# Performance work log

Hardware: AMD Instinct MI355X
Metric: run time of the kernel (lower is better)

Reference implementation:

```python
import math
import jax, jax.numpy as jnp
import numpy as np

SCALING = 16.0 / 32.0  # alpha / rank


def real_fourier_orthogonal_multiply(c):
    """Vectorized equivalent of the per-frequency Python loop: build a complex
    spectrum from real Fourier coefficients and inverse-rfft along last dim."""
    n = c.shape[-1]
    sqrt_n = math.sqrt(n)
    pair_scale = math.sqrt(n / 2.0)
    max_f = (n - 1) // 2
    work = c.astype(jnp.float32)
    dc = (work[..., 0] * sqrt_n)[..., None].astype(jnp.complex64)
    cos = work[..., 1:1 + 2 * max_f:2] * pair_scale
    sin = work[..., 2:2 + 2 * max_f:2] * pair_scale
    mid = (cos - 1j * sin).astype(jnp.complex64)  # freqs 1..max_f
    parts = [dc, mid]
    if n % 2 == 0:
        parts.append((work[..., -1] * sqrt_n)[..., None].astype(jnp.complex64))
    spectrum = jnp.concatenate(parts, axis=-1)  # [..., n//2+1]
    return jnp.fft.irfft(spectrum, n=n, axis=-1).astype(c.dtype)


def setup_inputs() -> dict:
    key = jax.random.key(0)
    ks = jax.random.split(key, 9)
    B, S, D_in, D_out, R0, R1, E = 4, 2048, 4096, 4096, 32, 8, 3
    x = jax.random.normal(ks[0], (B, S, D_in), dtype=jnp.float32)
    W_base = jax.random.normal(ks[1], (D_out, D_in), dtype=jnp.float32) * 0.02
    b_base = jax.random.normal(ks[2], (D_out,), dtype=jnp.float32) * 0.02
    enc0 = jax.random.normal(ks[3], (R0, D_in), dtype=jnp.float32) * 0.02
    enc1 = jax.random.normal(ks[4], (R1, D_in), dtype=jnp.float32) * 0.02
    coefs0 = jax.random.normal(ks[5], (E, D_out, R0), dtype=jnp.float32) * 0.02
    coefs1 = jax.random.normal(ks[6], (E, D_out, R1), dtype=jnp.float32) * 0.02
    # sparse decoder masks (buffers in the torch module)
    mask0 = jax.random.randint(ks[7], (E, D_out, R0), 0, 2).astype(bool)
    mask1 = jax.random.randint(ks[8], (E, D_out, R1), 0, 2).astype(bool)
    return dict(x=x, W_base=W_base, b_base=b_base, enc0=enc0, enc1=enc1,
                coefs0=coefs0, coefs1=coefs1, mask0=mask0, mask1=mask1)


def reference(x, W_base, b_base, enc0, enc1, coefs0, coefs1, mask0, mask1):
    # base linear
    base = jnp.einsum('bsd,od->bso', x, W_base) + b_base
    # encoder blocks (shared across experts)
    e0 = jnp.einsum('bsd,rd->bsr', x, enc0)  # [B,S,R0]
    e1 = jnp.einsum('bsd,rd->bsr', x, enc1)  # [B,S,R1]
    # masked decoder blocks per expert, summed over blocks
    w0 = coefs0 * mask0.astype(coefs0.dtype)  # [E,O,R0]
    w1 = coefs1 * mask1.astype(coefs1.dtype)  # [E,O,R1]
    decoded = (jnp.einsum('bsr,eor->ebso', e0, w0)
               + jnp.einsum('bsr,eor->ebso', e1, w1))  # [E,B,S,O]
    transformed = real_fourier_orthogonal_multiply(decoded)
    update = transformed.sum(axis=0)  # sum over active experts
    return base + update * SCALING
```

## Files before the change

kernel.cpp:

```cpp
#include <hip/hip_runtime.h>

typedef __attribute__((ext_vector_type(2))) float f32x2;
typedef __attribute__((ext_vector_type(4))) float f32x4;
typedef __attribute__((ext_vector_type(16))) float f32x16;
typedef __attribute__((ext_vector_type(8))) short bf16x8;
typedef __attribute__((ext_vector_type(8))) unsigned short u16x8;

#define GL2LDS(g, l) __builtin_amdgcn_global_load_lds( \
    (const __attribute__((address_space(1))) void*)(g), \
    (__attribute__((address_space(3))) void*)(l), 16, 0, 0)

__device__ __forceinline__ unsigned short f2bf(float x) {
    union { float f; unsigned u; } v; v.f = x;
    unsigned r = (v.u + 0x7FFF + ((v.u >> 16) & 1)) >> 16;
    return (unsigned short)r;
}

__global__ __launch_bounds__(256) void k_prep(const float* __restrict__ c0,
                                              const float* __restrict__ c1,
                                              const int* __restrict__ m0,
                                              const int* __restrict__ m1,
                                              float* __restrict__ Wc,
                                              const float* __restrict__ x,
                                              unsigned short* __restrict__ xb) {
    int b = blockIdx.x;
    if (b < 640) {
        int idx = b * 256 + threadIdx.x;
        if (idx >= 4096 * 40) return;
        int o = idx / 40, c = idx % 40;
        float s = 0.f;
        if (c < 32) {
            #pragma unroll
            for (int e = 0; e < 3; ++e) {
                int i = (e * 4096 + o) * 32 + c;
                s += c0[i] * (m0[i] != 0 ? 1.f : 0.f);
            }
        } else {
            int r = c - 32;
            #pragma unroll
            for (int e = 0; e < 3; ++e) {
                int i = (e * 4096 + o) * 8 + r;
                s += c1[i] * (m1[i] != 0 ? 1.f : 0.f);
            }
        }
        Wc[idx] = s;
    } else {
        int idx = (b - 640) * 256 + threadIdx.x;
        f32x4 f0 = ((const f32x4*)x)[(size_t)idx * 2];
        f32x4 f1 = ((const f32x4*)x)[(size_t)idx * 2 + 1];
        u16x8 o;
        o[0] = f2bf(f0[0]); o[1] = f2bf(f0[1]); o[2] = f2bf(f0[2]); o[3] = f2bf(f0[3]);
        o[4] = f2bf(f1[0]); o[5] = f2bf(f1[1]); o[6] = f2bf(f1[2]); o[7] = f2bf(f1[3]);
        *(u16x8*)(xb + (size_t)idx * 8) = o;
    }
}

__global__ __launch_bounds__(256) void k_gmat(const float* __restrict__ Wc,
                                              float* __restrict__ G) {
    __shared__ float lds[10752];
    int tid = threadIdx.x;
    int t_base = blockIdx.x * 8;
    int f_slot = tid & 31;
    int tg = (tid >> 5) & 1;
    int rg = tid >> 6;
    float acc[4][10];
    #pragma unroll
    for (int a = 0; a < 4; ++a)
        #pragma unroll
        for (int b = 0; b < 10; ++b) acc[a][b] = 0.f;

    for (int ch = 0; ch < 16; ++ch) {
        __syncthreads();
        #pragma unroll
        for (int j = 0; j < 10; ++j) {
            int idx = tid + j * 256;
            int row = idx / 20;
            int v = idx % 20;
            int f = ch * 128 + row;
            f32x4 val = {0.f, 0.f, 0.f, 0.f};
            if (f >= 1) val = *(const f32x4*)(Wc + (2 * f - 1) * 40 + v * 4);
            *(f32x4*)(lds + row * 84 + v * 4) = val;
        }
        __syncthreads();
        #pragma unroll
        for (int j2 = 0; j2 < 4; ++j2) {
            int f_local = f_slot + 32 * j2;
            int f = ch * 128 + f_local;
            float cs[4], sn[4];
            #pragma unroll
            for (int tt = 0; tt < 4; ++tt) {
                int t = t_base + tg * 4 + tt;
                int ph = (f * t) & 4095;
                float rev = (float)ph * (1.0f / 4096.0f);
                cs[tt] = __builtin_amdgcn_cosf(rev);
                sn[tt] = __builtin_amdgcn_sinf(rev);
            }
            const float* Lc = lds + f_local * 84 + rg * 10;
            const float* Ls = Lc + 40;
            #pragma unroll
            for (int rr = 0; rr < 10; ++rr) {
                float wc = Lc[rr], ws = Ls[rr];
                #pragma unroll
                for (int tt = 0; tt < 4; ++tt)
                    acc[tt][rr] += cs[tt] * wc + sn[tt] * ws;
            }
        }
    }
    __syncthreads();
    #pragma unroll
    for (int tt = 0; tt < 4; ++tt)
        #pragma unroll
        for (int rr = 0; rr < 10; ++rr)
            lds[tid * 40 + tt * 10 + rr] = acc[tt][rr];
    __syncthreads();
    for (int oi = tid; oi < 320; oi += 256) {
        int t_local = oi / 40, rc = oi % 40;
        int tg2 = t_local >> 2, tsub = t_local & 3;
        int rg2 = rc / 10, rsub = rc % 10;
        float s = 0.f;
        #pragma unroll
        for (int fs = 0; fs < 32; ++fs)
            s += lds[(fs + tg2 * 32 + rg2 * 64) * 40 + tsub * 10 + rsub];
        int t = t_base + t_local;
        float dc = Wc[rc];
        float ny = Wc[4095 * 40 + rc];
        float sign = (t & 1) ? -1.f : 1.f;
        float g = 0.5f * (0.0220970869120796f * s + (dc + sign * ny) * (1.0f / 64.0f));
        G[t * 40 + rc] = g;
    }
}

__global__ __launch_bounds__(256) void k_wcomb(const float* __restrict__ Wb,
                                               const float* __restrict__ enc0,
                                               const float* __restrict__ enc1,
                                               const float* __restrict__ G,
                                               unsigned short* __restrict__ Wcb) {
    __shared__ float ldsE[40 * 256];
    __shared__ float ldsG[32 * 40];
    int tid = threadIdx.x;
    int d0 = blockIdx.x * 256;
    int t0 = blockIdx.y * 32;
    #pragma unroll
    for (int j = 0; j < 10; ++j) {
        int idx = tid + j * 256;
        int k = idx / 64, v = idx % 64;
        const float* src = (k < 32) ? (enc0 + (size_t)k * 4096) : (enc1 + (size_t)(k - 32) * 4096);
        *(f32x4*)(ldsE + k * 256 + v * 4) = *(const f32x4*)(src + d0 + v * 4);
    }
    #pragma unroll
    for (int j = 0; j < 5; ++j) {
        int idx = tid + j * 256;
        ldsG[idx] = G[(size_t)(t0 + idx / 40) * 40 + (idx % 40)];
    }
    __syncthreads();
    int dg = tid & 31, tg = tid >> 5;
    f32x2 a[4][4];
    #pragma unroll
    for (int s = 0; s < 4; ++s)
        #pragma unroll
        for (int tt = 0; tt < 4; ++tt) a[s][tt] = (f32x2){0.f, 0.f};
    #pragma unroll 8
    for (int r = 0; r < 40; ++r) {
        f32x2 e[4];
        #pragma unroll
        for (int s = 0; s < 4; ++s)
            e[s] = *(const f32x2*)(ldsE + r * 256 + s * 64 + dg * 2);
        #pragma unroll
        for (int tt = 0; tt < 4; ++tt) {
            float g = ldsG[(tg * 4 + tt) * 40 + r];
            #pragma unroll
            for (int s = 0; s < 4; ++s)
                a[s][tt] += g * e[s];
        }
    }
    #pragma unroll
    for (int tt = 0; tt < 4; ++tt) {
        int t = t0 + tg * 4 + tt;
        #pragma unroll
        for (int s = 0; s < 4; ++s) {
            int d = d0 + s * 64 + dg * 2;
            f32x2 wv = *(const f32x2*)(Wb + (size_t)t * 4096 + d);
            f32x2 rv = a[s][tt] + wv;
            unsigned short lo = f2bf(rv[0]), hi = f2bf(rv[1]);
            *(unsigned*)(Wcb + (size_t)t * 4096 + d) = (unsigned)lo | ((unsigned)hi << 16);
        }
    }
}

__global__ __launch_bounds__(512, 2) void k_gemm(const unsigned short* __restrict__ A,
                                                 const unsigned short* __restrict__ B,
                                                 const float* __restrict__ bias,
                                                 float* __restrict__ C) {
    __shared__ __align__(16) short As[2][256 * 64];
    __shared__ __align__(16) short Bs[2][256 * 64];
    const int tid = threadIdx.x;
    const int lane = tid & 63, w = tid >> 6;
    const int wm = w >> 2, wn = w & 3;
    const int l15 = lane & 15;
    const int kc = lane >> 4;
    const int sk = lane & 7;

    int bid = blockIdx.x;
    int swz = (bid & 7) * 64 + (bid >> 3);
    int m0 = (swz >> 4) * 256;
    int n0 = (swz & 15) * 256;

    const int srow = w * 8 + (lane >> 3);
    const int scg  = (lane & 7) ^ ((lane >> 3) & 7);
    const unsigned short* Ag = A + (size_t)(m0 + srow) * 4096 + scg * 8;
    const unsigned short* Bg = B + (size_t)(n0 + srow) * 4096 + scg * 8;

#define STAGE(buf, kt) do { \
    _Pragma("unroll") \
    for (int c = 0; c < 4; ++c) { \
        GL2LDS(Ag + (size_t)(c * 64) * 4096 + (kt), &As[buf][(c * 64 + w * 8) * 64]); \
        GL2LDS(Bg + (size_t)(c * 64) * 4096 + (kt), &Bs[buf][(c * 64 + w * 8) * 64]); \
    } \
} while (0)

    int aoff[8], boff[4];
    #pragma unroll
    for (int mt = 0; mt < 8; ++mt) aoff[mt] = (wm * 128 + mt * 16 + l15) * 64;
    #pragma unroll
    for (int nt = 0; nt < 4; ++nt) boff[nt] = (wn * 64 + nt * 16 + l15) * 64;
    const int s0 = ((0 + kc) ^ sk) * 8;
    const int s1 = ((4 + kc) ^ sk) * 8;

    f32x4 acc[8][4];
    #pragma unroll
    for (int mt = 0; mt < 8; ++mt)
        #pragma unroll
        for (int nt = 0; nt < 4; ++nt)
            #pragma unroll
            for (int r = 0; r < 4; ++r) acc[mt][nt][r] = 0.f;

#define TILE_BODY(CB, kt, DO_STAGE, WAITK) do { \
    bf16x8 aF[8][2], bF[4][2]; \
    _Pragma("unroll") \
    for (int nt = 0; nt < 4; ++nt) \
        bF[nt][0] = *(const bf16x8*)&Bs[CB][boff[nt] + s0]; \
    _Pragma("unroll") \
    for (int mt = 0; mt < 8; ++mt) \
        aF[mt][0] = *(const bf16x8*)&As[CB][aoff[mt] + s0]; \
    _Pragma("unroll") \
    for (int nt = 0; nt < 4; ++nt) \
        bF[nt][1] = *(const bf16x8*)&Bs[CB][boff[nt] + s1]; \
    _Pragma("unroll") \
    for (int mt = 0; mt < 8; ++mt) \
        aF[mt][1] = *(const bf16x8*)&As[CB][aoff[mt] + s1]; \
    __builtin_amdgcn_s_setprio(1); \
    _Pragma("unroll") \
    for (int mt = 0; mt < 8; ++mt) \
        _Pragma("unroll") \
        for (int nt = 0; nt < 4; ++nt) \
            acc[mt][nt] = __builtin_amdgcn_mfma_f32_16x16x32_bf16(aF[mt][0], bF[nt][0], acc[mt][nt], 0, 0, 0); \
    __builtin_amdgcn_s_setprio(0); \
    asm volatile("s_waitcnt lgkmcnt(0)\n\ts_barrier" ::: "memory"); \
    if (DO_STAGE) STAGE(CB, (kt) + 128); \
    __builtin_amdgcn_s_setprio(1); \
    _Pragma("unroll") \
    for (int mt = 0; mt < 8; ++mt) \
        _Pragma("unroll") \
        for (int nt = 0; nt < 4; ++nt) \
            acc[mt][nt] = __builtin_amdgcn_mfma_f32_16x16x32_bf16(aF[mt][1], bF[nt][1], acc[mt][nt], 0, 0, 0); \
    __builtin_amdgcn_s_setprio(0); \
    if ((WAITK) == 8) { \
        asm volatile("s_waitcnt vmcnt(8)\n\ts_barrier" ::: "memory"); \
    } else if ((WAITK) == 0) { \
        asm volatile("s_waitcnt vmcnt(0)\n\ts_barrier" ::: "memory"); \
    } \
} while (0)

    STAGE(0, 0);
    STAGE(1, 64);
    asm volatile("s_waitcnt vmcnt(8)\n\ts_barrier" ::: "memory");

    for (int i = 0; i < 31; ++i) {
        int kt = i * 128;
        TILE_BODY(0, kt, true, 8);
        TILE_BODY(1, kt + 64, true, 8);
    }
    TILE_BODY(0, 62 * 64, false, 0);
    TILE_BODY(1, 63 * 64, false, -1);
#undef TILE_BODY
#undef STAGE

    const int r4 = (lane >> 4) * 4;
    float bv[4];
    #pragma unroll
    for (int nt = 0; nt < 4; ++nt) bv[nt] = bias[n0 + wn * 64 + nt * 16 + l15];
    #pragma unroll
    for (int mt = 0; mt < 8; ++mt) {
        #pragma unroll
        for (int nt = 0; nt < 4; ++nt) {
            #pragma unroll
            for (int r = 0; r < 4; ++r) {
                int row = m0 + wm * 128 + mt * 16 + r4 + r;
                C[(size_t)row * 4096 + n0 + wn * 64 + nt * 16 + l15] = acc[mt][nt][r] + bv[nt];
            }
        }
    }
}

extern "C" void kernel_launch(void* const* d_in, const int* in_sizes, int n_in,
                              void* d_out, int out_size, void* d_ws, size_t ws_size,
                              hipStream_t stream) {
    const float* x   = (const float*)d_in[0];
    const float* Wb  = (const float*)d_in[1];
    const float* bb  = (const float*)d_in[2];
    const float* e0  = (const float*)d_in[3];
    const float* e1  = (const float*)d_in[4];
    const float* c0  = (const float*)d_in[5];
    const float* c1  = (const float*)d_in[6];
    const int*   m0  = (const int*)d_in[7];
    const int*   m1  = (const int*)d_in[8];
    float* out = (float*)d_out;

    char* ws = (char*)d_ws;
    unsigned short* xb  = (unsigned short*)ws;
    float* Wc           = (float*)(ws + 67108864);
    float* G            = (float*)(ws + 67764224);
    unsigned short* Wcb = (unsigned short*)(ws + 68419584);

    k_prep <<<17024, 256, 0, stream>>>(c0, c1, m0, m1, Wc, x, xb);
    k_gmat <<<512, 256, 0, stream>>>(Wc, G);
    k_wcomb<<<dim3(16, 128), 256, 0, stream>>>(Wb, e0, e1, G, Wcb);
    k_gemm <<<512, 512, 0, stream>>>(xb, Wcb, bb, out);
}
```

Baseline: 600.7 us.

## Software-pipeline LDS fragment loads across tiles in GEMM main loop

Restructures the K-loop so the first-half A/B fragments of the next tile are read from LDS during the current tile, after the barrier, and overlap with the second-half MFMAs. Each tile now loads only its second-half fragments at the start, while the first-half MFMAs use fragments prefetched in the previous iteration. This aims to hide LDS read latency behind matrix math. The cost is more live registers for the two fragment sets, and the prefetch happens right after the vmcnt barrier, so the ordering has to stay correct.

```diff
diff --git a/kernel.cpp b/kernel.cpp
--- a/kernel.cpp
+++ b/kernel.cpp
@@ -234,54 +234,67 @@
             #pragma unroll
             for (int r = 0; r < 4; ++r) acc[mt][nt][r] = 0.f;
 
-#define TILE_BODY(CB, kt, DO_STAGE, WAITK) do { \
-    bf16x8 aF[8][2], bF[4][2]; \
+    bf16x8 fa0[8], fb0[4];
+    bf16x8 fa1[8], fb1[4];
+
+#define TILE_BODY(CB, NB, kt, DO_STAGE, WAITK, DO_NEXT) do { \
+     \
     _Pragma("unroll") \
     for (int nt = 0; nt < 4; ++nt) \
-        bF[nt][0] = *(const bf16x8*)&Bs[CB][boff[nt] + s0]; \
+        fb1[nt] = *(const bf16x8*)&Bs[CB][boff[nt] + s1]; \
     _Pragma("unroll") \
     for (int mt = 0; mt < 8; ++mt) \
-        aF[mt][0] = *(const bf16x8*)&As[CB][aoff[mt] + s0]; \
-    _Pragma("unroll") \
-    for (int nt = 0; nt < 4; ++nt) \
-        bF[nt][1] = *(const bf16x8*)&Bs[CB][boff[nt] + s1]; \
-    _Pragma("unroll") \
-    for (int mt = 0; mt < 8; ++mt) \
-        aF[mt][1] = *(const bf16x8*)&As[CB][aoff[mt] + s1]; \
+        fa1[mt] = *(const bf16x8*)&As[CB][aoff[mt] + s1]; \
     __builtin_amdgcn_s_setprio(1); \
     _Pragma("unroll") \
     for (int mt = 0; mt < 8; ++mt) \
         _Pragma("unroll") \
         for (int nt = 0; nt < 4; ++nt) \
-            acc[mt][nt] = __builtin_amdgcn_mfma_f32_16x16x32_bf16(aF[mt][0], bF[nt][0], acc[mt][nt], 0, 0, 0); \
+            acc[mt][nt] = __builtin_amdgcn_mfma_f32_16x16x32_bf16(fa0[mt], fb0[nt], acc[mt][nt], 0, 0, 0); \
     __builtin_amdgcn_s_setprio(0); \
+     \
     asm volatile("s_waitcnt lgkmcnt(0)\n\ts_barrier" ::: "memory"); \
     if (DO_STAGE) STAGE(CB, (kt) + 128); \
-    __builtin_amdgcn_s_setprio(1); \
-    _Pragma("unroll") \
-    for (int mt = 0; mt < 8; ++mt) \
-        _Pragma("unroll") \
-        for (int nt = 0; nt < 4; ++nt) \
-            acc[mt][nt] = __builtin_amdgcn_mfma_f32_16x16x32_bf16(aF[mt][1], bF[nt][1], acc[mt][nt], 0, 0, 0); \
-    __builtin_amdgcn_s_setprio(0); \
     if ((WAITK) == 8) { \
         asm volatile("s_waitcnt vmcnt(8)\n\ts_barrier" ::: "memory"); \
     } else if ((WAITK) == 0) { \
         asm volatile("s_waitcnt vmcnt(0)\n\ts_barrier" ::: "memory"); \
     } \
+     \
+    if (DO_NEXT) { \
+        _Pragma("unroll") \
+        for (int nt = 0; nt < 4; ++nt) \
+            fb0[nt] = *(const bf16x8*)&Bs[NB][boff[nt] + s0]; \
+        _Pragma("unroll") \
+        for (int mt = 0; mt < 8; ++mt) \
+            fa0[mt] = *(const bf16x8*)&As[NB][aoff[mt] + s0]; \
+    } \
+    __builtin_amdgcn_s_setprio(1); \
+    _Pragma("unroll") \
+    for (int mt = 0; mt < 8; ++mt) \
+        _Pragma("unroll") \
+        for (int nt = 0; nt < 4; ++nt) \
+            acc[mt][nt] = __builtin_amdgcn_mfma_f32_16x16x32_bf16(fa1[mt], fb1[nt], acc[mt][nt], 0, 0, 0); \
+    __builtin_amdgcn_s_setprio(0); \
 } while (0)
 
     STAGE(0, 0);
     STAGE(1, 64);
     asm volatile("s_waitcnt vmcnt(8)\n\ts_barrier" ::: "memory");
+    #pragma unroll
+    for (int nt = 0; nt < 4; ++nt)
+        fb0[nt] = *(const bf16x8*)&Bs[0][boff[nt] + s0];
+    #pragma unroll
+    for (int mt = 0; mt < 8; ++mt)
+        fa0[mt] = *(const bf16x8*)&As[0][aoff[mt] + s0];
 
     for (int i = 0; i < 31; ++i) {
         int kt = i * 128;
-        TILE_BODY(0, kt, true, 8);
-        TILE_BODY(1, kt + 64, true, 8);
-    }
-    TILE_BODY(0, 62 * 64, false, 0);
-    TILE_BODY(1, 63 * 64, false, -1);
+        TILE_BODY(0, 1, kt, true, 8, true);
+        TILE_BODY(1, 0, kt + 64, true, 8, true);
+    }
+    TILE_BODY(0, 1, 62 * 64, false, 0, true);
+    TILE_BODY(1, 0, 63 * 64, false, -1, false);
 #undef TILE_BODY
 #undef STAGE
 
```

Result: slower. 640.1 us (+6.6%).
